# Optimization experiments

Measured on AMD Instinct MI355X. Metric: run time of the kernel, lower is better.

Reference implementation:

```python
import jax, jax.numpy as jnp
import numpy as np

B, T, E = 64, 64, 512
D_MODEL = 2 * E          # 1024, mamba d_model (concat of spatial+temporal)
D_INNER = 2 * D_MODEL    # 2048
D_STATE = 16
DT_RANK = D_MODEL // 16  # 64
K_CONV = 4


def setup_inputs() -> dict:
    key = jax.random.key(0)
    ks = jax.random.split(key, 12)
    def n(k, shape, scale=0.02):
        return jax.random.normal(k, shape, jnp.float32) * scale
    return {
        "spatial_features": jax.random.normal(ks[0], (B, T, E), jnp.float32),
        "temporal_features": jax.random.normal(ks[1], (B, T, E), jnp.float32),
        "W_in": n(ks[2], (D_MODEL, 2 * D_INNER)),
        "conv_w": n(ks[3], (D_INNER, K_CONV)),
        "conv_b": jnp.zeros((D_INNER,), jnp.float32),
        "W_x": n(ks[4], (D_INNER, DT_RANK + 2 * D_STATE)),
        "W_dt": n(ks[5], (DT_RANK, D_INNER)),
        "b_dt": jnp.zeros((D_INNER,), jnp.float32),
        "A_log": n(ks[6], (D_INNER, D_STATE)),   # A = -exp(A_log) ~ -1
        "D_skip": jnp.ones((D_INNER,), jnp.float32),
        "W_out": n(ks[7], (D_INNER, D_MODEL)),
        "W1": n(ks[8], (D_MODEL, 512)),
        "b1": jnp.zeros((512,), jnp.float32),
        "W2": n(ks[9], (512, 256)),
        "b2": jnp.zeros((256,), jnp.float32),
        "W3": n(ks[10], (256, 6)),
        "b3": jnp.zeros((6,), jnp.float32),
    }


def _mamba(x, W_in, conv_w, conv_b, W_x, W_dt, b_dt, A_log, D_skip, W_out):
    # x: (B, T, d_model) -> (B, T, d_model). Standard Mamba selective-scan block.
    Bsz = x.shape[0]
    xz = jnp.einsum('btd,de->bte', x, W_in)            # (B,T,2*d_inner)
    xi, z = jnp.split(xz, 2, axis=-1)
    # causal depthwise conv1d over T
    xt = jnp.pad(jnp.swapaxes(xi, 1, 2), ((0, 0), (0, 0), (K_CONV - 1, 0)))
    conv = jax.lax.conv_general_dilated(
        xt, conv_w[:, None, :], (1,), 'VALID', feature_group_count=D_INNER)
    xc = jax.nn.silu(jnp.swapaxes(conv, 1, 2) + conv_b)  # (B,T,d_inner)
    proj = jnp.einsum('btd,de->bte', xc, W_x)            # (B,T,dt_rank+2n)
    dt_raw, Bs, Cs = jnp.split(proj, [DT_RANK, DT_RANK + D_STATE], axis=-1)
    dt = jax.nn.softplus(jnp.einsum('btr,rd->btd', dt_raw, W_dt) + b_dt)
    A = -jnp.exp(A_log)                                  # (d_inner, n)

    def step(h, inputs):
        dt_t, B_t, C_t, x_t = inputs                     # (B,d),(B,n),(B,n),(B,d)
        dA = jnp.exp(dt_t[..., None] * A)                # (B,d,n)
        h = dA * h + (dt_t * x_t)[..., None] * B_t[:, None, :]
        y = jnp.einsum('bdn,bn->bd', h, C_t)
        return h, y

    xs = (jnp.swapaxes(dt, 0, 1), jnp.swapaxes(Bs, 0, 1),
          jnp.swapaxes(Cs, 0, 1), jnp.swapaxes(xc, 0, 1))
    h0 = jnp.zeros((Bsz, D_INNER, D_STATE), xc.dtype)
    _, ys = jax.lax.scan(step, h0, xs)
    y = jnp.swapaxes(ys, 0, 1) + xc * D_skip
    y = y * jax.nn.silu(z)
    return jnp.einsum('btd,de->bte', y, W_out)


def reference(spatial_features, temporal_features, W_in, conv_w, conv_b, W_x,
              W_dt, b_dt, A_log, D_skip, W_out, W1, b1, W2, b2, W3, b3):
    # concat -> final Mamba -> per-frame MLP head (vectorized over B,T)
    x = jnp.concatenate([spatial_features, temporal_features], axis=-1)  # (B,T,2E)
    f = _mamba(x, W_in, conv_w, conv_b, W_x, W_dt, b_dt, A_log, D_skip, W_out)
    h1 = jax.nn.relu(f @ W1 + b1)
    h2 = jax.nn.relu(h1 @ W2 + b2)
    return h2 @ W3 + b3  # (B,T,6)
```

## Files before the change

kernel.cpp:

```cpp
#include <hip/hip_runtime.h>
#include <hip/hip_bf16.h>
#include <math.h>

#define B_   64
#define T_   64
#define E_   512
#define DM   1024
#define DI   2048
#define DS   16
#define DTR  64
#define M_   4096

typedef __hip_bfloat16 bf16;
typedef __attribute__((ext_vector_type(8))) short bf16x8;
typedef __attribute__((ext_vector_type(4))) float f32x4;

template<int SPLITK, int BM, int BN, int ATOMIC = 0>
__global__ __launch_bounds__(256) void gemm_mfma(
    const bf16* __restrict__ A, int lda,
    const bf16* __restrict__ Bt, int ldb,
    float* __restrict__ Cv, int ldc,
    int Ndim, int Kdim)
{
    __shared__ __align__(16) bf16 As[BM * 32];
    __shared__ __align__(16) bf16 Bs[BN * 32];
    const int tid  = threadIdx.x;
    const int wave = tid >> 6;
    const int lane = tid & 63;
    const int bm = blockIdx.y * BM;
    const int bn = blockIdx.x * BN;
    const int lrow = lane >> 2;
    const int lkc  = (lane & 3) * 8;
    constexpr int RPW = (BM + BN) / 4;
    constexpr int NI  = RPW / 16;
    constexpr int WMT = BM / 32;
    constexpr int WNT = BN / 32;
    const int wm = (wave >> 1) * (BM / 2);
    const int wn = (wave & 1) * (BN / 2);
    const int fm = lane & 15;
    const int fq = lane >> 4;

    int kstart = 0, kend = Kdim;
    if (SPLITK > 1) {
        int chunk = Kdim / SPLITK;
        kstart = blockIdx.z * chunk;
        kend = kstart + chunk;
    }

    f32x4 acc[WMT][WNT];
    #pragma unroll
    for (int i = 0; i < WMT; ++i)
        #pragma unroll
        for (int j = 0; j < WNT; ++j)
            acc[i][j] = (f32x4){0.f, 0.f, 0.f, 0.f};

    for (int k0 = kstart; k0 < kend; k0 += 32) {
        #pragma unroll
        for (int i = 0; i < NI; ++i) {
            int rowbase = wave * RPW + i * 16;
            int row = rowbase + lrow;
            if (rowbase < BM) {
                const bf16* ga = A + (size_t)(bm + row) * lda + k0 + lkc;
                __builtin_amdgcn_global_load_lds(
                    (const __attribute__((address_space(1))) void*)ga,
                    (__attribute__((address_space(3))) void*)&As[rowbase * 32],
                    16, 0, 0);
            } else {
                int brow = bn + row - BM;
                if (brow >= Ndim) brow = Ndim - 1;
                const bf16* gb = Bt + (size_t)brow * ldb + k0 + lkc;
                __builtin_amdgcn_global_load_lds(
                    (const __attribute__((address_space(1))) void*)gb,
                    (__attribute__((address_space(3))) void*)&Bs[(rowbase - BM) * 32],
                    16, 0, 0);
            }
        }
        __syncthreads();
        bf16x8 a[WMT], b[WNT];
        #pragma unroll
        for (int i = 0; i < WMT; ++i)
            a[i] = *(const bf16x8*)&As[(wm + i * 16 + fm) * 32 + fq * 8];
        #pragma unroll
        for (int j = 0; j < WNT; ++j)
            b[j] = *(const bf16x8*)&Bs[(wn + j * 16 + fm) * 32 + fq * 8];
        #pragma unroll
        for (int i = 0; i < WMT; ++i)
            #pragma unroll
            for (int j = 0; j < WNT; ++j)
                acc[i][j] = __builtin_amdgcn_mfma_f32_16x16x32_bf16(
                    a[i], b[j], acc[i][j], 0, 0, 0);
        __syncthreads();
    }

    size_t zoff = (SPLITK > 1 && !ATOMIC) ? (size_t)blockIdx.z * M_ * ldc : 0;
    #pragma unroll
    for (int i = 0; i < WMT; ++i) {
        int rowb = bm + wm + i * 16 + fq * 4;
        #pragma unroll
        for (int j = 0; j < WNT; ++j) {
            int col = bn + wn + j * 16 + fm;
            if (col < Ndim) {
                #pragma unroll
                for (int r = 0; r < 4; ++r) {
                    float v = acc[i][j][r];
                    size_t off = (size_t)(rowb + r) * ldc + col;
                    if (ATOMIC) atomicAdd(&Cv[off], v);
                    else        Cv[zoff + off] = v;
                }
            }
        }
    }
}

__global__ __launch_bounds__(256) void gemm_g1_conv(
    const bf16* __restrict__ A,
    const bf16* __restrict__ Bt,
    bf16* __restrict__ xcb,
    bf16* __restrict__ zb,
    const float* __restrict__ conv_w,
    const float* __restrict__ conv_b,
    const bf16* __restrict__ W1T,
    const bf16* __restrict__ Wob,
    bf16* __restrict__ WcT)
{
    constexpr int XS = 136;
    __shared__ __align__(16) bf16 smem[128 * XS];
    const int tid  = threadIdx.x;
    const int wave = tid >> 6;
    const int lane = tid & 63;
    const int lrow = lane >> 2;
    const int lkc  = (lane & 3) * 8;
    const int wm = (wave >> 1) * 64;
    const int fm = lane & 15;
    const int fq = lane >> 4;

    if (blockIdx.x >= 32) {
        const int fbm = (blockIdx.x - 32) * 128;
        const int fbn = blockIdx.y * 64;
        const int fwn = (wave & 1) * 32;
        f32x4 facc[4][2];
        #pragma unroll
        for (int i = 0; i < 4; ++i)
            #pragma unroll
            for (int j = 0; j < 2; ++j)
                facc[i][j] = (f32x4){0.f, 0.f, 0.f, 0.f};

        for (int k0 = 0; k0 < 1024; k0 += 32) {
            #pragma unroll
            for (int i = 0; i < 3; ++i) {
                int rowbase = wave * 48 + i * 16;
                int row = rowbase + lrow;
                if (rowbase < 128) {
                    const bf16* ga = W1T + (size_t)(fbm + row) * 1024 + k0 + lkc;
                    __builtin_amdgcn_global_load_lds(
                        (const __attribute__((address_space(1))) void*)ga,
                        (__attribute__((address_space(3))) void*)&smem[rowbase * 32],
                        16, 0, 0);
                } else {
                    const bf16* gb = Wob + (size_t)(fbn + row - 128) * 1024 + k0 + lkc;
                    __builtin_amdgcn_global_load_lds(
                        (const __attribute__((address_space(1))) void*)gb,
                        (__attribute__((address_space(3))) void*)&smem[4096 + (rowbase - 128) * 32],
                        16, 0, 0);
                }
            }
            __syncthreads();
            bf16x8 a[4], b[2];
            #pragma unroll
            for (int i = 0; i < 4; ++i)
                a[i] = *(const bf16x8*)&smem[(wm + i * 16 + fm) * 32 + fq * 8];
            #pragma unroll
            for (int j = 0; j < 2; ++j)
                b[j] = *(const bf16x8*)&smem[4096 + (fwn + j * 16 + fm) * 32 + fq * 8];
            #pragma unroll
            for (int i = 0; i < 4; ++i)
                #pragma unroll
                for (int j = 0; j < 2; ++j)
                    facc[i][j] = __builtin_amdgcn_mfma_f32_16x16x32_bf16(
                        a[i], b[j], facc[i][j], 0, 0, 0);
            __syncthreads();
        }
        #pragma unroll
        for (int i = 0; i < 4; ++i) {
            int rowb = fbm + wm + i * 16 + fq * 4;
            #pragma unroll
            for (int j = 0; j < 2; ++j) {
                int col = fbn + fwn + j * 16 + fm;
                #pragma unroll
                for (int r = 0; r < 4; ++r)
                    WcT[(size_t)(rowb + r) * 2048 + col] =
                        __float2bfloat16(facc[i][j][r]);
            }
        }
        return;
    }

    const int bm = blockIdx.y * 128;
    const int bn = blockIdx.x * 128;
    const int wn = (wave & 1) * 64;

    f32x4 acc[4][4];
    #pragma unroll
    for (int i = 0; i < 4; ++i)
        #pragma unroll
        for (int j = 0; j < 4; ++j)
            acc[i][j] = (f32x4){0.f, 0.f, 0.f, 0.f};

    for (int k0 = 0; k0 < 1024; k0 += 32) {
        #pragma unroll
        for (int i = 0; i < 4; ++i) {
            int rowbase = wave * 64 + i * 16;
            int row = rowbase + lrow;
            if (rowbase < 128) {
                const bf16* ga = A + (size_t)(bm + row) * 1024 + k0 + lkc;
                __builtin_amdgcn_global_load_lds(
                    (const __attribute__((address_space(1))) void*)ga,
                    (__attribute__((address_space(3))) void*)&smem[rowbase * 32],
                    16, 0, 0);
            } else {
                const bf16* gb = Bt + (size_t)(bn + row - 128) * 1024 + k0 + lkc;
                __builtin_amdgcn_global_load_lds(
                    (const __attribute__((address_space(1))) void*)gb,
                    (__attribute__((address_space(3))) void*)&smem[4096 + (rowbase - 128) * 32],
                    16, 0, 0);
            }
        }
        __syncthreads();
        bf16x8 a[4], b[4];
        #pragma unroll
        for (int i = 0; i < 4; ++i)
            a[i] = *(const bf16x8*)&smem[(wm + i * 16 + fm) * 32 + fq * 8];
        #pragma unroll
        for (int j = 0; j < 4; ++j)
            b[j] = *(const bf16x8*)&smem[4096 + (wn + j * 16 + fm) * 32 + fq * 8];
        #pragma unroll
        for (int i = 0; i < 4; ++i)
            #pragma unroll
            for (int j = 0; j < 4; ++j)
                acc[i][j] = __builtin_amdgcn_mfma_f32_16x16x32_bf16(
                    a[i], b[j], acc[i][j], 0, 0, 0);
        __syncthreads();
    }

    if (bn < 2048) {
        #pragma unroll
        for (int i = 0; i < 4; ++i) {
            int rowb = wm + i * 16 + fq * 4;
            #pragma unroll
            for (int j = 0; j < 4; ++j) {
                int col = wn + j * 16 + fm;
                #pragma unroll
                for (int r = 0; r < 4; ++r)
                    smem[(rowb + r) * XS + col] = __float2bfloat16(acc[i][j][r]);
            }
        }
        __syncthreads();
        {
            int col = tid & 127;
            int seq = tid >> 7;
            int gcol = bn + col;
            float4 cw = *(const float4*)&conv_w[gcol * 4];
            float cb = conv_b[gcol];
            float w0 = 0.f, w1 = 0.f, w2 = 0.f;
            int base = seq * 64;
            for (int t = 0; t < 64; ++t) {
                int idx = (base + t) * XS + col;
                float cur = __bfloat162float(smem[idx]);
                float cacc = cb;
                cacc = fmaf(w0, cw.x, cacc); cacc = fmaf(w1, cw.y, cacc);
                cacc = fmaf(w2, cw.z, cacc); cacc = fmaf(cur, cw.w, cacc);
                smem[idx] = __float2bfloat16(__fdividef(cacc, 1.f + __expf(-cacc)));
                w0 = w1; w1 = w2; w2 = cur;
            }
        }
        __syncthreads();
        #pragma unroll
        for (int it = 0; it < 8; ++it) {
            int g = it * 256 + tid;
            int row = g >> 4;
            int cg = (g & 15) * 8;
            bf16x8 v = *(const bf16x8*)&smem[row * XS + cg];
            *(bf16x8*)&xcb[(size_t)(bm + row) * 2048 + bn + cg] = v;
        }
    } else {
        #pragma unroll
        for (int i = 0; i < 4; ++i) {
            int rowb = bm + wm + i * 16 + fq * 4;
            #pragma unroll
            for (int j = 0; j < 4; ++j) {
                int col = bn - 2048 + wn + j * 16 + fm;
                #pragma unroll
                for (int r = 0; r < 4; ++r)
                    zb[(size_t)(rowb + r) * 2048 + col] =
                        __float2bfloat16(acc[i][j][r]);
            }
        }
    }
}

__global__ __launch_bounds__(256) void scan_g3_kernel(
    const float* __restrict__ proj,
    const bf16*  __restrict__ WdT,
    const float* __restrict__ b_dt,
    bf16* __restrict__ xcy,
    const bf16*  __restrict__ zb,
    const float* __restrict__ A_log,
    const float* __restrict__ D_skip)
{
    __shared__ float BC[64][32];
    __shared__ __align__(16) bf16 Adt[64 * 64];
    __shared__ __align__(16) bf16 Bdt[256 * 64];
    const int tid  = threadIdx.x;
    const int wave = tid >> 6;
    const int lane = tid & 63;
    const int b  = blockIdx.y;
    const int dg = blockIdx.x;
    const int fm = lane & 15;
    const int fq = lane >> 4;

    for (int i = tid; i < 64 * 32; i += 256) {
        int t = i >> 5, c = i & 31;
        BC[t][c] = proj[(size_t)(b * 64 + t) * 96 + 64 + c];
    }
    {
        int arow = tid >> 2;
        int ak = (tid & 3) * 16;
        const float* ga = proj + (size_t)(b * 64 + arow) * 96 + ak;
        float4 v0 = *(const float4*)(ga + 0);
        float4 v1 = *(const float4*)(ga + 4);
        float4 v2 = *(const float4*)(ga + 8);
        float4 v3 = *(const float4*)(ga + 12);
        bf16 o[16] = {
            __float2bfloat16(v0.x), __float2bfloat16(v0.y),
            __float2bfloat16(v0.z), __float2bfloat16(v0.w),
            __float2bfloat16(v1.x), __float2bfloat16(v1.y),
            __float2bfloat16(v1.z), __float2bfloat16(v1.w),
            __float2bfloat16(v2.x), __float2bfloat16(v2.y),
            __float2bfloat16(v2.z), __float2bfloat16(v2.w),
            __float2bfloat16(v3.x), __float2bfloat16(v3.y),
            __float2bfloat16(v3.z), __float2bfloat16(v3.w)};
        *(bf16x8*)&Adt[arow * 64 + ak]     = *(const bf16x8*)&o[0];
        *(bf16x8*)&Adt[arow * 64 + ak + 8] = *(const bf16x8*)&o[8];
    }
    #pragma unroll
    for (int i = 0; i < 8; ++i) {
        int rowbase = wave * 64 + i * 8;
        const bf16* gb = WdT + (size_t)(dg * 256 + rowbase + (lane >> 3)) * 64
                             + (lane & 7) * 8;
        __builtin_amdgcn_global_load_lds(
            (const __attribute__((address_space(1))) void*)gb,
            (__attribute__((address_space(3))) void*)&Bdt[rowbase * 64],
            16, 0, 0);
    }
    __syncthreads();

    f32x4 acc[4][4];
    #pragma unroll
    for (int i = 0; i < 4; ++i)
        #pragma unroll
        for (int j = 0; j < 4; ++j)
            acc[i][j] = (f32x4){0.f, 0.f, 0.f, 0.f};
    #pragma unroll
    for (int k0 = 0; k0 < 64; k0 += 32) {
        bf16x8 a[4], bfr[4];
        #pragma unroll
        for (int i = 0; i < 4; ++i)
            a[i] = *(const bf16x8*)&Adt[(i * 16 + fm) * 64 + k0 + fq * 8];
        #pragma unroll
        for (int j = 0; j < 4; ++j)
            bfr[j] = *(const bf16x8*)&Bdt[(wave * 64 + j * 16 + fm) * 64 + k0 + fq * 8];
        #pragma unroll
        for (int i = 0; i < 4; ++i)
            #pragma unroll
            for (int j = 0; j < 4; ++j)
                acc[i][j] = __builtin_amdgcn_mfma_f32_16x16x32_bf16(
                    a[i], bfr[j], acc[i][j], 0, 0, 0);
    }
    __syncthreads();
    bf16* dt_s = Bdt;
    #pragma unroll
    for (int j = 0; j < 4; ++j) {
        int dloc = wave * 64 + j * 16 + fm;
        float bv = b_dt[dg * 256 + dloc];
        #pragma unroll
        for (int i = 0; i < 4; ++i) {
            #pragma unroll
            for (int r = 0; r < 4; ++r) {
                int t = i * 16 + fq * 4 + r;
                float v = acc[i][j][r] + bv;
                v = (v > 20.f) ? v : __logf(1.f + __expf(v));
                dt_s[t * 256 + dloc] = __float2bfloat16(v);
            }
        }
    }
    __syncthreads();

    const int d = dg * 256 + tid;
    float av[16];
    const float4* alp = (const float4*)(A_log + d * 16);
    *(float4*)&av[0]  = alp[0];
    *(float4*)&av[4]  = alp[1];
    *(float4*)&av[8]  = alp[2];
    *(float4*)&av[12] = alp[3];
    float A[16];
    #pragma unroll
    for (int n = 0; n < 16; ++n) A[n] = -__expf(av[n]);
    const float Dv = D_skip[d];
    float h[16];
    #pragma unroll
    for (int n = 0; n < 16; ++n) h[n] = 0.f;

    #pragma unroll 2
    for (int t = 0; t < T_; ++t) {
        int row = b * T_ + t;
        size_t off = (size_t)row * DI + d;
        float xv = __bfloat162float(xcy[off]);
        float dt = __bfloat162float(dt_s[t * 256 + tid]);
        float dtx = dt * xv;
        float y = 0.f;
        #pragma unroll
        for (int n = 0; n < 16; ++n) {
            float dA = __expf(dt * A[n]);
            h[n] = fmaf(dA, h[n], dtx * BC[t][n]);
            y = fmaf(h[n], BC[t][16 + n], y);
        }
        float sk = fmaf(xv, Dv, y);
        float z = __bfloat162float(zb[off]);
        float g = __fdividef(z, 1.f + __expf(-z));
        xcy[off] = __float2bfloat16(sk * g);
    }
}

__global__ __launch_bounds__(256) void gemm_g6(
    const float* __restrict__ p5,
    const bf16* __restrict__ W2T,
    float* __restrict__ p6,
    const float* __restrict__ b1)
{
    __shared__ __align__(16) bf16 As[128 * 32];
    __shared__ __align__(16) bf16 Bs[128 * 32];
    const int tid  = threadIdx.x;
    const int wave = tid >> 6;
    const int lane = tid & 63;
    const int bm = blockIdx.y * 128;
    const int bn = blockIdx.x * 128;
    const int lrow = lane >> 2;
    const int lkc  = (lane & 3) * 8;
    const int wm = (wave >> 1) * 64;
    const int wn = (wave & 1) * 64;
    const int fm = lane & 15;
    const int fq = lane >> 4;
    const int kstart = blockIdx.z * 128;

    f32x4 acc[4][4];
    #pragma unroll
    for (int i = 0; i < 4; ++i)
        #pragma unroll
        for (int j = 0; j < 4; ++j)
            acc[i][j] = (f32x4){0.f, 0.f, 0.f, 0.f};

    for (int k0 = kstart; k0 < kstart + 128; k0 += 32) {
        #pragma unroll
        for (int i = 0; i < 2; ++i) {
            int rowbase = wave * 32 + i * 16;
            const bf16* gb = W2T + (size_t)(bn + rowbase + lrow) * 512 + k0 + lkc;
            __builtin_amdgcn_global_load_lds(
                (const __attribute__((address_space(1))) void*)gb,
                (__attribute__((address_space(3))) void*)&Bs[rowbase * 32],
                16, 0, 0);
        }
        #pragma unroll
        for (int p = 0; p < 4; ++p) {
            int idx = p * 256 + tid;
            int arow = idx >> 3;
            int ak4 = (idx & 7) * 4;
            const float* ga = p5 + (size_t)(bm + arow) * 512 + k0 + ak4;
            float4 u = *(const float4*)ga;
            float4 v = *(const float4*)(ga + 2097152);
            float4 bb = *(const float4*)(b1 + k0 + ak4);
            bf16 o[4] = {
                __float2bfloat16(fmaxf(u.x + v.x + bb.x, 0.f)),
                __float2bfloat16(fmaxf(u.y + v.y + bb.y, 0.f)),
                __float2bfloat16(fmaxf(u.z + v.z + bb.z, 0.f)),
                __float2bfloat16(fmaxf(u.w + v.w + bb.w, 0.f))};
            *(short4*)&As[arow * 32 + ak4] = *(const short4*)o;
        }
        __syncthreads();
        bf16x8 a[4], b[4];
        #pragma unroll
        for (int i = 0; i < 4; ++i)
            a[i] = *(const bf16x8*)&As[(wm + i * 16 + fm) * 32 + fq * 8];
        #pragma unroll
        for (int j = 0; j < 4; ++j)
            b[j] = *(const bf16x8*)&Bs[(wn + j * 16 + fm) * 32 + fq * 8];
        #pragma unroll
        for (int i = 0; i < 4; ++i)
            #pragma unroll
            for (int j = 0; j < 4; ++j)
                acc[i][j] = __builtin_amdgcn_mfma_f32_16x16x32_bf16(
                    a[i], b[j], acc[i][j], 0, 0, 0);
        __syncthreads();
    }

    size_t zoff = (size_t)blockIdx.z * M_ * 256;
    #pragma unroll
    for (int i = 0; i < 4; ++i) {
        int rowb = bm + wm + i * 16 + fq * 4;
        #pragma unroll
        for (int j = 0; j < 4; ++j) {
            int col = bn + wn + j * 16 + fm;
            #pragma unroll
            for (int r = 0; r < 4; ++r)
                p6[zoff + (size_t)(rowb + r) * 256 + col] = acc[i][j][r];
        }
    }
}

__global__ __launch_bounds__(256) void prep_kernel(
    const float* __restrict__ sp, const float* __restrict__ tp,
    bf16* __restrict__ xb, float* __restrict__ proj,
    const float* __restrict__ W_in,  bf16* __restrict__ WinT,
    const float* __restrict__ W_out, bf16* __restrict__ Wob,
    const float* __restrict__ W_x,   bf16* __restrict__ WxT,
    const float* __restrict__ W_dt,  bf16* __restrict__ WdT,
    const float* __restrict__ W1,    bf16* __restrict__ W1T,
    const float* __restrict__ W2,    bf16* __restrict__ W2T)
{
    __shared__ float tile[32][33];
    const int b = blockIdx.x;
    const int tid = threadIdx.x;
    if (b < 4096) {
        int idx = b * 256 + tid;
        int row = idx >> 8;
        int c4 = (idx & 255) * 4;
        const float* src = (c4 < 512) ? (sp + (size_t)row * 512 + c4)
                                      : (tp + (size_t)row * 512 + (c4 - 512));
        float4 v = *(const float4*)src;
        bf16* dst = xb + (size_t)row * 1024 + c4;
        dst[0] = __float2bfloat16(v.x); dst[1] = __float2bfloat16(v.y);
        dst[2] = __float2bfloat16(v.z); dst[3] = __float2bfloat16(v.w);
        if (idx < 98304)
            *(float4*)(proj + (size_t)idx * 4) = make_float4(0.f, 0.f, 0.f, 0.f);
        return;
    }
    if (b < 6144) {
        int idx = (b - 4096) * 1024 + tid * 4;
        float4 v = *(const float4*)(W_out + idx);
        bf16 o[4] = {__float2bfloat16(v.x), __float2bfloat16(v.y),
                     __float2bfloat16(v.z), __float2bfloat16(v.w)};
        *(short4*)&Wob[idx] = *(short4*)o;
        return;
    }
    const float* W; bf16* Wt; int K, N, tb;
    if      (b < 6336) { W = W_x;  Wt = WxT;  K = 2048; N = 96;   tb = b - 6144; }
    else if (b < 6464) { W = W_dt; Wt = WdT;  K = 64;   N = 2048; tb = b - 6336; }
    else if (b < 6976) { W = W1;   Wt = W1T;  K = 1024; N = 512;  tb = b - 6464; }
    else if (b < 7104) { W = W2;   Wt = W2T;  K = 512;  N = 256;  tb = b - 6976; }
    else               { W = W_in; Wt = WinT; K = 1024; N = 4096; tb = b - 7104; }
    int nb = N / 32;
    int bn = (tb % nb) * 32, bk = (tb / nb) * 32;
    int tx = tid & 31, ty = tid >> 5;
    #pragma unroll
    for (int i = 0; i < 32; i += 8)
        tile[ty + i][tx] = W[(size_t)(bk + ty + i) * N + bn + tx];
    __syncthreads();
    #pragma unroll
    for (int i = 0; i < 32; i += 8)
        Wt[(size_t)(bn + ty + i) * K + bk + tx] = __float2bfloat16(tile[tx][ty + i]);
}

template<int P>
__global__ __launch_bounds__(256) void head_kernel(
    const float* __restrict__ p6, int stride,
    const float* __restrict__ b2,
    const float* __restrict__ W3, const float* __restrict__ b3,
    float* __restrict__ out)
{
    int row = blockIdx.x * 4 + (threadIdx.x >> 6);
    int lane = threadIdx.x & 63;
    float acc[6] = {0.f, 0.f, 0.f, 0.f, 0.f, 0.f};
    #pragma unroll
    for (int kk = 0; kk < 4; ++kk) {
        int c = lane + kk * 64;
        size_t off = (size_t)row * 256 + c;
        float s = p6[off];
        #pragma unroll
        for (int p = 1; p < P; ++p) s += p6[(size_t)p * stride + off];
        s = fmaxf(s + b2[c], 0.f);
        #pragma unroll
        for (int n = 0; n < 6; ++n) acc[n] = fmaf(s, W3[c * 6 + n], acc[n]);
    }
    #pragma unroll
    for (int n = 0; n < 6; ++n) {
        float v = acc[n];
        #pragma unroll
        for (int off = 32; off > 0; off >>= 1) v += __shfl_down(v, off);
        if (lane == 0) out[(size_t)row * 6 + n] = v + b3[n];
    }
}

extern "C" void kernel_launch(void* const* d_in, const int* in_sizes, int n_in,
                              void* d_out, int out_size, void* d_ws, size_t ws_size,
                              hipStream_t stream)
{
    const float* spatial  = (const float*)d_in[0];
    const float* temporal = (const float*)d_in[1];
    const float* W_in     = (const float*)d_in[2];
    const float* conv_w   = (const float*)d_in[3];
    const float* conv_b   = (const float*)d_in[4];
    const float* W_x      = (const float*)d_in[5];
    const float* W_dt     = (const float*)d_in[6];
    const float* b_dt     = (const float*)d_in[7];
    const float* A_log    = (const float*)d_in[8];
    const float* D_skip   = (const float*)d_in[9];
    const float* W_out    = (const float*)d_in[10];
    const float* W1       = (const float*)d_in[11];
    const float* b1       = (const float*)d_in[12];
    const float* W2       = (const float*)d_in[13];
    const float* b2       = (const float*)d_in[14];
    const float* W3       = (const float*)d_in[15];
    const float* b3       = (const float*)d_in[16];
    float* out = (float*)d_out;

    char* w = (char*)d_ws;
    bf16*  xcb  = (bf16*)(w);
    bf16*  zb   = (bf16*)(w + 16777216);
    float* p5   = (float*)(w + 33554432);
    float* p6   = (float*)(w + 50331648);
    bf16*  xb   = (bf16*)(w + 67108864);
    bf16*  WinT = (bf16*)(w + 75497472);
    bf16*  WcT  = (bf16*)(w + 83886080);
    bf16*  W1T  = (bf16*)(w + 85983232);
    bf16*  W2T  = (bf16*)(w + 87031808);
    bf16*  WxT  = (bf16*)(w + 87293952);
    bf16*  WdT  = (bf16*)(w + 87687168);
    float* proj = (float*)(w + 87949312);
    bf16*  Wob  = (bf16*)(w + 89522176);

    dim3 blk(256);

    prep_kernel<<<dim3(11200), blk, 0, stream>>>(
        spatial, temporal, xb, proj, W_in, WinT, W_out, Wob,
        W_x, WxT, W_dt, WdT, W1, W1T, W2, W2T);

    gemm_g1_conv<<<dim3(36, 32), blk, 0, stream>>>(
        xb, WinT, xcb, zb, conv_w, conv_b, W1T, Wob, WcT);

    gemm_mfma<8, 128, 128, 1><<<dim3(1, 32, 8), blk, 0, stream>>>(
        xcb, 2048, WxT, 2048, proj, 96, 96, 2048);

    scan_g3_kernel<<<dim3(8, 64), blk, 0, stream>>>(
        proj, WdT, b_dt, xcb, zb, A_log, D_skip);

    gemm_mfma<2, 128, 128><<<dim3(4, 32, 2), blk, 0, stream>>>(
        xcb, 2048, WcT, 2048, p5, 512, 512, 2048);

    gemm_g6<<<dim3(2, 32, 4), blk, 0, stream>>>(p5, W2T, p6, b1);

    head_kernel<4><<<dim3(1024), blk, 0, stream>>>(
        p6, 1048576, b2, W3, b3, out);
}
```

Before: 277.7 us.

## Fuse x_proj GEMM into conv epilogue and raise split-K for fused out/W1 GEMM

Computes the xc·W_x projection directly inside the conv kernel's epilogue from the freshly produced xc tile still in shared memory. Each block accumulates its 128-column K-slice into proj with atomics, which removes the separate split-K launch and its re-read of xcb. It also raises split-K of the W_out·W1 GEMM from 2 to 4, with gemm_g6 summing four partials, and moves p6 to reuse the xb buffer. The cost is more atomic traffic into proj, heavier conv blocks, and more partial-sum memory traffic.

```diff
diff --git a/kernel.cpp b/kernel.cpp
--- a/kernel.cpp
+++ b/kernel.cpp
@@ -15,7 +15,7 @@
 typedef __attribute__((ext_vector_type(8))) short bf16x8;
 typedef __attribute__((ext_vector_type(4))) float f32x4;
 
-template<int SPLITK, int BM, int BN, int ATOMIC = 0>
+template<int SPLITK, int BM, int BN>
 __global__ __launch_bounds__(256) void gemm_mfma(
     const bf16* __restrict__ A, int lda,
     const bf16* __restrict__ Bt, int ldb,
@@ -92,7 +92,7 @@
         __syncthreads();
     }
 
-    size_t zoff = (SPLITK > 1 && !ATOMIC) ? (size_t)blockIdx.z * M_ * ldc : 0;
+    size_t zoff = (SPLITK > 1) ? (size_t)blockIdx.z * M_ * ldc : 0;
     #pragma unroll
     for (int i = 0; i < WMT; ++i) {
         int rowb = bm + wm + i * 16 + fq * 4;
@@ -101,12 +101,8 @@
             int col = bn + wn + j * 16 + fm;
             if (col < Ndim) {
                 #pragma unroll
-                for (int r = 0; r < 4; ++r) {
-                    float v = acc[i][j][r];
-                    size_t off = (size_t)(rowb + r) * ldc + col;
-                    if (ATOMIC) atomicAdd(&Cv[off], v);
-                    else        Cv[zoff + off] = v;
-                }
+                for (int r = 0; r < 4; ++r)
+                    Cv[zoff + (size_t)(rowb + r) * ldc + col] = acc[i][j][r];
             }
         }
     }
@@ -121,7 +117,9 @@
     const float* __restrict__ conv_b,
     const bf16* __restrict__ W1T,
     const bf16* __restrict__ Wob,
-    bf16* __restrict__ WcT)
+    bf16* __restrict__ WcT,
+    const bf16* __restrict__ WxT,
+    float* __restrict__ proj)
 {
     constexpr int XS = 136;
     __shared__ __align__(16) bf16 smem[128 * XS];
@@ -281,6 +279,45 @@
             int cg = (g & 15) * 8;
             bf16x8 v = *(const bf16x8*)&smem[row * XS + cg];
             *(bf16x8*)&xcb[(size_t)(bm + row) * 2048 + bn + cg] = v;
+        }
+        {
+            const int mw = wave * 32;
+            f32x4 dacc[2][6];
+            #pragma unroll
+            for (int i = 0; i < 2; ++i)
+                #pragma unroll
+                for (int j = 0; j < 6; ++j)
+                    dacc[i][j] = (f32x4){0.f, 0.f, 0.f, 0.f};
+            #pragma unroll
+            for (int kit = 0; kit < 4; ++kit) {
+                bf16x8 bfrag[6], afrag[2];
+                #pragma unroll
+                for (int j = 0; j < 6; ++j)
+                    bfrag[j] = *(const bf16x8*)(WxT
+                        + (size_t)(j * 16 + fm) * 2048 + bn + kit * 32 + fq * 8);
+                #pragma unroll
+                for (int i = 0; i < 2; ++i)
+                    afrag[i] = *(const bf16x8*)&smem[
+                        (mw + i * 16 + fm) * XS + kit * 32 + fq * 8];
+                #pragma unroll
+                for (int i = 0; i < 2; ++i)
+                    #pragma unroll
+                    for (int j = 0; j < 6; ++j)
+                        dacc[i][j] = __builtin_amdgcn_mfma_f32_16x16x32_bf16(
+                            afrag[i], bfrag[j], dacc[i][j], 0, 0, 0);
+            }
+            #pragma unroll
+            for (int i = 0; i < 2; ++i) {
+                int rowb = bm + mw + i * 16 + fq * 4;
+                #pragma unroll
+                for (int j = 0; j < 6; ++j) {
+                    int n = j * 16 + fm;
+                    #pragma unroll
+                    for (int r = 0; r < 4; ++r)
+                        atomicAdd(&proj[(size_t)(rowb + r) * 96 + n],
+                                  dacc[i][j][r]);
+                }
+            }
         }
     } else {
         #pragma unroll
@@ -475,14 +512,16 @@
             int arow = idx >> 3;
             int ak4 = (idx & 7) * 4;
             const float* ga = p5 + (size_t)(bm + arow) * 512 + k0 + ak4;
-            float4 u = *(const float4*)ga;
-            float4 v = *(const float4*)(ga + 2097152);
+            float4 u0 = *(const float4*)ga;
+            float4 u1 = *(const float4*)(ga + 2097152);
+            float4 u2 = *(const float4*)(ga + 4194304);
+            float4 u3 = *(const float4*)(ga + 6291456);
             float4 bb = *(const float4*)(b1 + k0 + ak4);
             bf16 o[4] = {
-                __float2bfloat16(fmaxf(u.x + v.x + bb.x, 0.f)),
-                __float2bfloat16(fmaxf(u.y + v.y + bb.y, 0.f)),
-                __float2bfloat16(fmaxf(u.z + v.z + bb.z, 0.f)),
-                __float2bfloat16(fmaxf(u.w + v.w + bb.w, 0.f))};
+                __float2bfloat16(fmaxf(u0.x + u1.x + u2.x + u3.x + bb.x, 0.f)),
+                __float2bfloat16(fmaxf(u0.y + u1.y + u2.y + u3.y + bb.y, 0.f)),
+                __float2bfloat16(fmaxf(u0.z + u1.z + u2.z + u3.z + bb.z, 0.f)),
+                __float2bfloat16(fmaxf(u0.w + u1.w + u2.w + u3.w + bb.w, 0.f))};
             *(short4*)&As[arow * 32 + ak4] = *(const short4*)o;
         }
         __syncthreads();
@@ -626,9 +665,9 @@
     bf16*  xcb  = (bf16*)(w);
     bf16*  zb   = (bf16*)(w + 16777216);
     float* p5   = (float*)(w + 33554432);
-    float* p6   = (float*)(w + 50331648);
     bf16*  xb   = (bf16*)(w + 67108864);
     bf16*  WinT = (bf16*)(w + 75497472);
+    float* p6   = (float*)(w + 67108864);
     bf16*  WcT  = (bf16*)(w + 83886080);
     bf16*  W1T  = (bf16*)(w + 85983232);
     bf16*  W2T  = (bf16*)(w + 87031808);
@@ -644,15 +683,12 @@
         W_x, WxT, W_dt, WdT, W1, W1T, W2, W2T);
 
     gemm_g1_conv<<<dim3(36, 32), blk, 0, stream>>>(
-        xb, WinT, xcb, zb, conv_w, conv_b, W1T, Wob, WcT);
-
-    gemm_mfma<8, 128, 128, 1><<<dim3(1, 32, 8), blk, 0, stream>>>(
-        xcb, 2048, WxT, 2048, proj, 96, 96, 2048);
+        xb, WinT, xcb, zb, conv_w, conv_b, W1T, Wob, WcT, WxT, proj);
 
     scan_g3_kernel<<<dim3(8, 64), blk, 0, stream>>>(
         proj, WdT, b_dt, xcb, zb, A_log, D_skip);
 
-    gemm_mfma<2, 128, 128><<<dim3(4, 32, 2), blk, 0, stream>>>(
+    gemm_mfma<4, 128, 128><<<dim3(4, 32, 4), blk, 0, stream>>>(
         xcb, 2048, WcT, 2048, p5, 512, 512, 2048);
 
     gemm_g6<<<dim3(2, 32, 4), blk, 0, stream>>>(p5, W2T, p6, b1);
```

After: 274.4 us. Within noise of the previous version (-1.2%).
